# Performance work log

Measured on AMD Instinct MI355X. Metric: run time of the kernel, lower is better.

Reference implementation:

```python
import jax, jax.numpy as jnp
import numpy as np

D_MODEL = 256
MLP_DIM = 1024
EPS = 1e-5

def _layernorm(x, g, b):
    mu = jnp.mean(x, axis=-1, keepdims=True)
    var = jnp.mean(jnp.square(x - mu), axis=-1, keepdims=True)
    return (x - mu) * jax.lax.rsqrt(var + EPS) * g + b

def setup_inputs() -> dict:
    key = jax.random.key(0)
    ks = jax.random.split(key, 4)
    d, m = D_MODEL, MLP_DIM
    x = jax.random.normal(ks[0], (8, 1024, 4, d), dtype=jnp.float32)
    w_qkv = jax.random.normal(ks[1], (3 * d, d), dtype=jnp.float32) * 0.05  # torch Linear weight (out,in)
    gamma1 = jnp.ones((d,), jnp.float32)
    beta1 = jnp.zeros((d,), jnp.float32)
    gamma2 = jnp.ones((d,), jnp.float32)
    beta2 = jnp.zeros((d,), jnp.float32)
    w1 = jax.random.normal(ks[2], (m, d), dtype=jnp.float32) * 0.05
    b1 = jnp.zeros((m,), jnp.float32)
    w2 = jax.random.normal(ks[3], (d, m), dtype=jnp.float32) * 0.05
    b2 = jnp.zeros((d,), jnp.float32)
    return {"x": x, "w_qkv": w_qkv, "gamma1": gamma1, "beta1": beta1,
            "gamma2": gamma2, "beta2": beta2, "w1": w1, "b1": b1, "w2": w2, "b2": b2}

def reference(x, w_qkv, gamma1, beta1, gamma2, beta2, w1, b1, w2, b2):
    bsz, n, h, d = x.shape
    scale = d ** -0.5
    # --- attention branch: x + attn(norm1(x)) ---
    xn = _layernorm(x, gamma1, beta1)
    # Linear(d, 3d): xn @ W^T, then reshape trailing 3d -> (d, 3) as in torch
    qkv = jnp.einsum('bnhd,ed->bnhe', xn, w_qkv).reshape(bsz, n * h, d, 3)
    q, k, v = qkv[..., 0], qkv[..., 1], qkv[..., 2]   # [b, n*h, d]
    dots = jnp.einsum('bid,bjd->bij', q, k) * scale   # [b, n*h, n*h]
    attn = jax.nn.softmax(dots, axis=-1)              # dropout=0 -> identity
    out = jnp.einsum('bij,bjd->bid', attn, v).reshape(bsz, n, h, d)
    x = x + out
    # --- mlp branch: x + mlp(norm2(x)) ---
    xn2 = _layernorm(x, gamma2, beta2)
    hid = jax.nn.silu(jnp.einsum('bnhd,md->bnhm', xn2, w1) + b1)
    x = x + jnp.einsum('bnhm,dm->bnhd', hid, w2) + b2
    return x
```

## Files before the change

### kernel.cpp

```cpp
#include <hip/hip_runtime.h>


typedef __attribute__((ext_vector_type(8))) short bf16x8;
typedef __attribute__((ext_vector_type(4))) short bf16x4;
typedef __attribute__((ext_vector_type(4))) float f32x4;
typedef __attribute__((ext_vector_type(16))) float f32x16;

static __device__ __forceinline__ short f2bf(float f) {
    union { float f; unsigned u; } v; v.f = f;
    unsigned r = (v.u + 0x7FFFu + ((v.u >> 16) & 1u)) >> 16;
    return (short)r;
}

static __device__ __forceinline__ void gll16(const void* g, void* l) {
    __builtin_amdgcn_global_load_lds(
        (const __attribute__((address_space(1))) unsigned*)g,
        (__attribute__((address_space(3))) unsigned*)l, 16, 0, 0);
}

__global__ __launch_bounds__(256) void k_cvt(const float* __restrict__ wqkv,
                                             const float* __restrict__ w1,
                                             const float* __restrict__ w2,
                                             short* __restrict__ owqkv,
                                             short* __restrict__ ow1,
                                             short* __restrict__ ow2) {
    int i = blockIdx.x * 256 + threadIdx.x;
    if (i < 196608) {
        int e = i >> 8, col = i & 255;
        int dd = e / 3, which = e - dd * 3;
        float v = wqkv[i];
        if (which == 0) v *= 0.0625f * 1.44269504f;
        owqkv[((which << 8) + dd) * 256 + col] = f2bf(v);
    }
    if (i < 262144) { ow1[i] = f2bf(w1[i]); ow2[i] = f2bf(w2[i]); }
}

__global__ __launch_bounds__(256) void k_ln(const float* __restrict__ x,
                                            const float* __restrict__ g,
                                            const float* __restrict__ bta,
                                            short* __restrict__ out) {
    int w = threadIdx.x >> 6, lane = threadIdx.x & 63;
    long row = (long)blockIdx.x * 4 + w;
    float4 v = *((const float4*)(x + row * 256) + lane);
    float s = v.x + v.y + v.z + v.w;
    float q = v.x * v.x + v.y * v.y + v.z * v.z + v.w * v.w;
    for (int off = 1; off < 64; off <<= 1) {
        s += __shfl_xor(s, off);
        q += __shfl_xor(q, off);
    }
    float mean = s * (1.0f / 256.0f);
    float var = q * (1.0f / 256.0f) - mean * mean;
    float rstd = rsqrtf(var + 1e-5f);
    float4 gg = *((const float4*)g + lane);
    float4 bb = *((const float4*)bta + lane);
    short4 o;
    o.x = f2bf((v.x - mean) * rstd * gg.x + bb.x);
    o.y = f2bf((v.y - mean) * rstd * gg.y + bb.y);
    o.z = f2bf((v.z - mean) * rstd * gg.z + bb.z);
    o.w = f2bf((v.w - mean) * rstd * gg.w + bb.w);
    *((short4*)(out + row * 256) + lane) = o;
}

__global__ __launch_bounds__(512, 2) void k_qkv(const short* __restrict__ xn,
                                                const short* __restrict__ wb,
                                                short* __restrict__ Q,
                                                short* __restrict__ K,
                                                short* __restrict__ VT) {
    __shared__ __attribute__((aligned(16))) short lds_b[2][64 * 256];
    __shared__ __attribute__((aligned(16))) short lds_t[64 * 136];
    int t = threadIdx.x, w = t >> 6, l = t & 63, l5 = l & 31;
    int ln = l & 15, qd = l >> 4;
    int m0 = blockIdx.x * 128;
    int moff = (w >> 1) * 32, noff = (w & 1) * 32;

    bf16x8 af[2][8];
    #pragma unroll
    for (int mi = 0; mi < 2; mi++)
        #pragma unroll
        for (int kc = 0; kc < 8; kc++)
            af[mi][kc] = *(const bf16x8*)(xn + (long)(m0 + moff + mi * 16 + ln) * 256 + kc * 32 + qd * 8);

    int boff[4], blds[4];
    #pragma unroll
    for (int i = 0; i < 4; i++) {
        int r = w * 8 + i * 2 + (l >> 5);
        boff[i] = r * 512 + ((l5 ^ (r & 31)) * 16);
        blds[i] = (w * 8 + i * 2) * 512;
    }
    const char* gB = (const char*)wb;
    #pragma unroll
    for (int i = 0; i < 4; i++) gll16(gB + boff[i], (char*)lds_b[0] + blds[i]);
    __syncthreads();

    for (int nt = 0; nt < 12; nt++) {
        int cur = nt & 1;
        if (nt < 11) {
            long base = (long)(nt + 1) * 32768;
            #pragma unroll
            for (int i = 0; i < 4; i++)
                gll16(gB + base + boff[i], (char*)lds_b[cur ^ 1] + blds[i]);
        }
        const char* lb = (const char*)lds_b[cur];
        f32x4 acc[2][2] = {};
        #pragma unroll
        for (int ks = 0; ks < 8; ks++) {
            int ca = ks * 4 + qd;
            int rb0 = noff + ln, rb1 = noff + 16 + ln;
            bf16x8 b0 = *(const bf16x8*)(lb + rb0 * 512 + ((ca ^ (rb0 & 31)) * 16));
            bf16x8 b1 = *(const bf16x8*)(lb + rb1 * 512 + ((ca ^ (rb1 & 31)) * 16));
            acc[0][0] = __builtin_amdgcn_mfma_f32_16x16x32_bf16(af[0][ks], b0, acc[0][0], 0, 0, 0);
            acc[0][1] = __builtin_amdgcn_mfma_f32_16x16x32_bf16(af[0][ks], b1, acc[0][1], 0, 0, 0);
            acc[1][0] = __builtin_amdgcn_mfma_f32_16x16x32_bf16(af[1][ks], b0, acc[1][0], 0, 0, 0);
            acc[1][1] = __builtin_amdgcn_mfma_f32_16x16x32_bf16(af[1][ks], b1, acc[1][1], 0, 0, 0);
        }
        int e0 = nt * 64;
        if (e0 < 512) {
            #pragma unroll
            for (int mi = 0; mi < 2; mi++)
                #pragma unroll
                for (int nj = 0; nj < 2; nj++)
                    #pragma unroll
                    for (int rg = 0; rg < 4; rg++) {
                        int gr = m0 + moff + mi * 16 + qd * 4 + rg;
                        int e = e0 + noff + nj * 16 + ln;
                        short bv = f2bf(acc[mi][nj][rg]);
                        if (e < 256) Q[(long)gr * 256 + e] = bv;
                        else K[(long)gr * 256 + (e - 256)] = bv;
                    }
        } else {
            #pragma unroll
            for (int mi = 0; mi < 2; mi++)
                #pragma unroll
                for (int nj = 0; nj < 2; nj++)
                    #pragma unroll
                    for (int rg = 0; rg < 4; rg++) {
                        int dl = noff + nj * 16 + ln;
                        int il = moff + mi * 16 + qd * 4 + rg;
                        lds_t[dl * 136 + il] = f2bf(acc[mi][nj][rg]);
                    }
            __syncthreads();
            int bb = m0 >> 12, i0 = m0 & 4095;
            int dl = t >> 3, ch = t & 7;
            const int4* s4 = (const int4*)(lds_t + dl * 136 + ch * 16);
            int4 v0 = s4[0], v1 = s4[1];
            long vrow = ((long)(bb * 256 + (e0 - 512) + dl)) * 4096 + i0 + ch * 16;
            *(int4*)(VT + vrow) = v0;
            *(int4*)(VT + vrow + 8) = v1;
        }
        __syncthreads();
    }
}

__global__ __launch_bounds__(512, 2) void k_attn(const short* __restrict__ Q,
                                                 const short* __restrict__ K,
                                                 const short* __restrict__ VT,
                                                 const float* __restrict__ x,
                                                 float* __restrict__ out) {
    __shared__ __attribute__((aligned(16))) short lds_k[2][64 * 256];
    __shared__ __attribute__((aligned(16))) short lds_v[2][2][256 * 40];
    int t = threadIdx.x, w = t >> 6, l = t & 63, l5 = l & 31, h = l >> 5;
    int ww = w & 3, hkv = w >> 2;
    int b = blockIdx.x;
    int q0 = blockIdx.y * 128 + ww * 32;

    bf16x8 qf[16];
    {
        const short* qrow = Q + ((long)(b * 4096 + q0 + l5)) * 256;
        #pragma unroll
        for (int kc = 0; kc < 16; kc++) qf[kc] = *(const bf16x8*)(qrow + kc * 16 + h * 8);
    }
    f32x16 O[8] = {};
    float lsum = 0.f;

    const char* Kb = (const char*)(K + (long)b * 4096 * 256);
    const int4* gv = (const int4*)(VT + (long)b * 4096 * 256);

    int koff[4], klds[4];
    #pragma unroll
    for (int i = 0; i < 4; i++) {
        int r = w * 8 + i * 2 + (l >> 5);
        koff[i] = r * 512 + ((l5 ^ (r & 31)) * 16);
        klds[i] = (w * 8 + i * 2) * 512;
    }
    int vgbase[4], vloff[4];
    #pragma unroll
    for (int i = 0; i < 4; i++) {
        int c = t + 512 * i;
        int sub = c >> 10, cc = c & 1023, d = cc >> 2, ch = cc & 3;
        vgbase[i] = d * 512 + sub * 4 + ch;
        vloff[i] = sub * 20480 + d * 80 + ch * 16;
    }
    int4 vs[4];

    #pragma unroll
    for (int i = 0; i < 4; i++) vs[i] = gv[vgbase[i]];
    #pragma unroll
    for (int i = 0; i < 4; i++) gll16(Kb + koff[i], (char*)lds_k[0] + klds[i]);
    #pragma unroll
    for (int i = 0; i < 4; i++)
        *(int4*)((char*)lds_v + vloff[i]) = vs[i];
    __syncthreads();

    const char* lvmine = (const char*)lds_v + hkv * 20480;

    for (int jt = 0; jt < 64; jt++) {
        int cur = jt & 1;
        if (jt < 63) {
            #pragma unroll
            for (int i = 0; i < 4; i++) vs[i] = gv[vgbase[i] + (jt + 1) * 8];
            int ka = (jt + 1) * 32768;
            #pragma unroll
            for (int i = 0; i < 4; i++)
                gll16(Kb + ka + koff[i], (char*)lds_k[cur ^ 1] + klds[i]);
        }
        const short* lk = lds_k[cur] + hkv * 32 * 256;
        const char* lv = lvmine + cur * 40960;
        f32x16 st = {};
        #pragma unroll
        for (int kc = 0; kc < 16; kc++) {
            int cc = kc * 2 + h;
            bf16x8 a = *(const bf16x8*)(lk + (l5 * 32 + (cc ^ l5)) * 8);
            st = __builtin_amdgcn_mfma_f32_32x32x16_bf16(a, qf[kc], st, 0, 0, 0);
        }
        unsigned pw[4][2];
        #pragma unroll
        for (int r4 = 0; r4 < 4; r4++) {
            float p0 = __builtin_amdgcn_exp2f(st[r4 * 4 + 0]);
            float p1 = __builtin_amdgcn_exp2f(st[r4 * 4 + 1]);
            float p2 = __builtin_amdgcn_exp2f(st[r4 * 4 + 2]);
            float p3 = __builtin_amdgcn_exp2f(st[r4 * 4 + 3]);
            lsum += (p0 + p1) + (p2 + p3);
            union { float f; unsigned u; } u0, u1, u2, u3;
            u0.f = p0; u1.f = p1; u2.f = p2; u3.f = p3;
            pw[r4][0] = __builtin_amdgcn_perm(u1.u + 0x8000u, u0.u + 0x8000u, 0x07060302u);
            pw[r4][1] = __builtin_amdgcn_perm(u3.u + 0x8000u, u2.u + 0x8000u, 0x07060302u);
        }
        bf16x8 pfr[2];
        #pragma unroll
        for (int k2 = 0; k2 < 2; k2++) {
            unsigned a0 = pw[2 * k2][0], a1 = pw[2 * k2][1];
            unsigned b0 = pw[2 * k2 + 1][0], b1 = pw[2 * k2 + 1][1];
            asm("v_permlane32_swap_b32 %0, %1" : "+v"(a0), "+v"(b0));
            asm("v_permlane32_swap_b32 %0, %1" : "+v"(a1), "+v"(b1));
            union { unsigned u[4]; bf16x8 v; } f;
            f.u[0] = a0; f.u[1] = a1; f.u[2] = b0; f.u[3] = b1;
            pfr[k2] = f.v;
        }
        if (jt < 63) {
            #pragma unroll
            for (int i = 0; i < 4; i++)
                *(int4*)((char*)lds_v + (cur ^ 1) * 40960 + vloff[i]) = vs[i];
        }
        #pragma unroll
        for (int dt = 0; dt < 8; dt++) {
            const char* vbase = lv + (dt * 32 + l5) * 80;
            #pragma unroll
            for (int k2 = 0; k2 < 2; k2++) {
                bf16x8 va = *(const bf16x8*)(vbase + (k2 * 2 + h) * 16);
                O[dt] = __builtin_amdgcn_mfma_f32_32x32x16_bf16(va, pfr[k2], O[dt], 0, 0, 0);
            }
        }
        __syncthreads();
    }

    float lt = lsum + __shfl_xor(lsum, 32);
    float* lmrg = (float*)&lds_v[1][0][0];
    lmrg[hkv * 128 + ww * 32 + l5] = lt;
    __syncthreads();
    float ltot = lmrg[ww * 32 + l5] + lmrg[128 + ww * 32 + l5];
    float rinv = 1.0f / ltot;

    float* omrg = (float*)&lds_v[0][0][0];
    float* fscr = (float*)lds_k[0] + ww * (32 * 33);
    #pragma unroll
    for (int dt = 0; dt < 8; dt++) {
        if (hkv == 1) {
            #pragma unroll
            for (int r = 0; r < 16; r++) omrg[ww * 1024 + r * 64 + l] = O[dt][r];
        }
        __syncthreads();
        if (hkv == 0) {
            #pragma unroll
            for (int r = 0; r < 16; r++) {
                float Om = O[dt][r] + omrg[ww * 1024 + r * 64 + l];
                int drow = (r & 3) + 8 * (r >> 2) + 4 * h;
                fscr[drow * 33 + l5] = Om * rinv;
            }
            asm volatile("s_waitcnt lgkmcnt(0)" ::: "memory");
            #pragma unroll
            for (int it = 0; it < 16; it++) {
                int ql = it * 2 + h;
                float v = fscr[l5 * 33 + ql];
                long idx = ((long)(b * 4096 + q0 + ql)) * 256 + dt * 32 + l5;
                out[idx] = x[idx] + v;
            }
            asm volatile("s_waitcnt lgkmcnt(0)" ::: "memory");
        }
        __syncthreads();
    }
}

__global__ __launch_bounds__(256, 2) void k_mlp(const short* __restrict__ xn,
                                                const short* __restrict__ w1b,
                                                const short* __restrict__ w2b,
                                                const float* __restrict__ b1,
                                                const float* __restrict__ b2,
                                                float* __restrict__ out) {
    __shared__ __attribute__((aligned(16))) short lds_w[2][32 * 256];
    __shared__ __attribute__((aligned(16))) short lds_h[64 * 264];
    int t = threadIdx.x, w = t >> 6, l = t & 63, l5 = l & 31, ln = l & 15, qd = l >> 4;
    int R0 = blockIdx.x * 64;
    int mrow = (w & 1) * 32, colh = (w >> 1) * 16;
    int lr = colh + ln;

    long s1off[4], s2off[4]; int wlds[4];
    #pragma unroll
    for (int i = 0; i < 4; i++) {
        int r = w * 8 + i * 2 + (l >> 5);
        int ch = l5 ^ (r & 31);
        s1off[i] = (long)r * 512 + ch * 16;
        s2off[i] = (long)r * 2048 + ch * 16;
        wlds[i] = (w * 8 + i * 2) * 512;
    }
    const char* W1c = (const char*)w1b;
    const char* W2c = (const char*)w2b;

    f32x4 Oc[8][2] = {};
    #pragma unroll
    for (int i = 0; i < 4; i++)
        gll16(W1c + s1off[i], (char*)lds_w[0] + wlds[i]);
    __syncthreads();
    int cur = 0;

    for (int pass = 0; pass < 4; pass++) {
        bf16x8 a1f[2][8];
        #pragma unroll
        for (int mi = 0; mi < 2; mi++)
            #pragma unroll
            for (int kc = 0; kc < 8; kc++)
                a1f[mi][kc] = *(const bf16x8*)(xn + (long)(R0 + mrow + mi * 16 + ln) * 256 + kc * 32 + qd * 8);
        #pragma unroll
        for (int nt = 0; nt < 8; nt++) {
            if (nt < 7) {
                long base = (long)(pass * 256 + (nt + 1) * 32) * 512;
                #pragma unroll
                for (int i = 0; i < 4; i++)
                    gll16(W1c + base + s1off[i], (char*)lds_w[cur ^ 1] + wlds[i]);
            } else {
                long base = (long)pass * 512;
                #pragma unroll
                for (int i = 0; i < 4; i++)
                    gll16(W2c + base + s2off[i], (char*)lds_w[cur ^ 1] + wlds[i]);
            }
            const short* lw = lds_w[cur];
            f32x4 acc[2] = {};
            #pragma unroll
            for (int kc = 0; kc < 8; kc++) {
                int cc = kc * 4 + qd;
                bf16x8 bf = *(const bf16x8*)(lw + lr * 256 + (cc ^ lr) * 8);
                acc[0] = __builtin_amdgcn_mfma_f32_16x16x32_bf16(a1f[0][kc], bf, acc[0], 0, 0, 0);
                acc[1] = __builtin_amdgcn_mfma_f32_16x16x32_bf16(a1f[1][kc], bf, acc[1], 0, 0, 0);
            }
            float bb = b1[pass * 256 + nt * 32 + lr];
            #pragma unroll
            for (int mi = 0; mi < 2; mi++)
                #pragma unroll
                for (int rg = 0; rg < 4; rg++) {
                    float z = acc[mi][rg] + bb;
                    float sv = z / (1.0f + __expf(-z));
                    lds_h[(mrow + mi * 16 + qd * 4 + rg) * 264 + nt * 32 + lr] = f2bf(sv);
                }
            __syncthreads();
            cur ^= 1;
        }
        bf16x8 a2f[2][8];
        #pragma unroll
        for (int mi = 0; mi < 2; mi++)
            #pragma unroll
            for (int kc = 0; kc < 8; kc++)
                a2f[mi][kc] = *(const bf16x8*)&lds_h[(mrow + mi * 16 + ln) * 264 + kc * 32 + qd * 8];
        #pragma unroll
        for (int nt = 0; nt < 8; nt++) {
            if (nt < 7) {
                long base = (long)((nt + 1) * 32) * 2048 + (long)pass * 512;
                #pragma unroll
                for (int i = 0; i < 4; i++)
                    gll16(W2c + base + s2off[i], (char*)lds_w[cur ^ 1] + wlds[i]);
            } else if (pass < 3) {
                long base = (long)((pass + 1) * 256) * 512;
                #pragma unroll
                for (int i = 0; i < 4; i++)
                    gll16(W1c + base + s1off[i], (char*)lds_w[cur ^ 1] + wlds[i]);
            }
            const short* lw = lds_w[cur];
            #pragma unroll
            for (int kc = 0; kc < 8; kc++) {
                int cc = kc * 4 + qd;
                bf16x8 bf = *(const bf16x8*)(lw + lr * 256 + (cc ^ lr) * 8);
                Oc[nt][0] = __builtin_amdgcn_mfma_f32_16x16x32_bf16(a2f[0][kc], bf, Oc[nt][0], 0, 0, 0);
                Oc[nt][1] = __builtin_amdgcn_mfma_f32_16x16x32_bf16(a2f[1][kc], bf, Oc[nt][1], 0, 0, 0);
            }
            __syncthreads();
            cur ^= 1;
        }
    }
    #pragma unroll
    for (int nt = 0; nt < 8; nt++) {
        int dd = nt * 32 + lr;
        float bb = b2[dd];
        #pragma unroll
        for (int mi = 0; mi < 2; mi++)
            #pragma unroll
            for (int rg = 0; rg < 4; rg++) {
                long idx = (long)(R0 + mrow + mi * 16 + qd * 4 + rg) * 256 + dd;
                out[idx] = out[idx] + Oc[nt][mi][rg] + bb;
            }
    }
}

extern "C" void kernel_launch(void* const* d_in, const int* in_sizes, int n_in,
                              void* d_out, int out_size, void* d_ws, size_t ws_size,
                              hipStream_t stream) {
    const float* x    = (const float*)d_in[0];
    const float* wqkv = (const float*)d_in[1];
    const float* g1   = (const float*)d_in[2];
    const float* be1  = (const float*)d_in[3];
    const float* g2   = (const float*)d_in[4];
    const float* be2  = (const float*)d_in[5];
    const float* w1   = (const float*)d_in[6];
    const float* b1   = (const float*)d_in[7];
    const float* w2   = (const float*)d_in[8];
    const float* b2   = (const float*)d_in[9];
    float* out = (float*)d_out;
    char* ws = (char*)d_ws;
    short* WQKV = (short*)(ws);
    short* W1B  = (short*)(ws + (512l << 10));
    short* W2B  = (short*)(ws + (1l << 20));
    short* XN   = (short*)(ws + (2l << 20));
    short* Qb   = (short*)(ws + (18l << 20));
    short* Kb   = (short*)(ws + (34l << 20));
    short* VTb  = (short*)(ws + (50l << 20));

    k_cvt<<<1024, 256, 0, stream>>>(wqkv, w1, w2, WQKV, W1B, W2B);
    k_ln<<<8192, 256, 0, stream>>>(x, g1, be1, XN);
    k_qkv<<<256, 512, 0, stream>>>(XN, WQKV, Qb, Kb, VTb);
    k_attn<<<dim3(8, 32), 512, 0, stream>>>(Qb, Kb, VTb, x, out);
    k_ln<<<8192, 256, 0, stream>>>(out, g2, be2, XN);
    k_mlp<<<512, 256, 0, stream>>>(XN, W1B, W2B, b1, b2, out);
}
```

Baseline: 399.3 us.

## Fuse layernorms into QKV and MLP kernels, drop standalone LN launches

Removes the two k_ln kernels and the bf16 normalized-activation buffer. The QKV and MLP kernels now read fp32 rows directly, compute mean and rstd per row with cross-lane shuffles, and build the bf16 A-fragments in registers. The intent is to cut two launches and the write-then-read of the normalized tensor. In exchange each GEMM block reads fp32 input twice (stats pass, then normalize pass) and uses more registers. The MLP A-fragments are also loaded once before the pass loop instead of once per pass.

Result: slower. 415.2 us (+4.0%).

```diff
diff --git a/kernel.cpp b/kernel.cpp
--- a/kernel.cpp
+++ b/kernel.cpp
@@ -16,6 +16,55 @@
     __builtin_amdgcn_global_load_lds(
         (const __attribute__((address_space(1))) unsigned*)g,
         (__attribute__((address_space(3))) unsigned*)l, 16, 0, 0);
+}
+
+static __device__ __forceinline__ void ln_frags(const float* __restrict__ xin,
+                                                const float* __restrict__ g,
+                                                const float* __restrict__ be,
+                                                long r0, int ln, int qd,
+                                                bf16x8 af[2][8]) {
+    float mean[2], rstd[2];
+    #pragma unroll
+    for (int mi = 0; mi < 2; mi++) {
+        const float* xr = xin + (r0 + mi * 16 + ln) * 256 + qd * 8;
+        float s = 0.f, qq = 0.f;
+        #pragma unroll
+        for (int kc = 0; kc < 8; kc++) {
+            float4 lo = *(const float4*)(xr + kc * 32);
+            float4 hi = *(const float4*)(xr + kc * 32 + 4);
+            s += (lo.x + lo.y) + (lo.z + lo.w) + (hi.x + hi.y) + (hi.z + hi.w);
+            qq += lo.x * lo.x + lo.y * lo.y + lo.z * lo.z + lo.w * lo.w
+                + hi.x * hi.x + hi.y * hi.y + hi.z * hi.z + hi.w * hi.w;
+        }
+        s += __shfl_xor(s, 16); s += __shfl_xor(s, 32);
+        qq += __shfl_xor(qq, 16); qq += __shfl_xor(qq, 32);
+        mean[mi] = s * (1.0f / 256.0f);
+        float var = qq * (1.0f / 256.0f) - mean[mi] * mean[mi];
+        rstd[mi] = rsqrtf(var + 1e-5f);
+    }
+    #pragma unroll
+    for (int mi = 0; mi < 2; mi++) {
+        const float* xr = xin + (r0 + mi * 16 + ln) * 256 + qd * 8;
+        #pragma unroll
+        for (int kc = 0; kc < 8; kc++) {
+            float4 lo = *(const float4*)(xr + kc * 32);
+            float4 hi = *(const float4*)(xr + kc * 32 + 4);
+            float4 glo = *(const float4*)(g + kc * 32 + qd * 8);
+            float4 ghi = *(const float4*)(g + kc * 32 + qd * 8 + 4);
+            float4 blo = *(const float4*)(be + kc * 32 + qd * 8);
+            float4 bhi = *(const float4*)(be + kc * 32 + qd * 8 + 4);
+            union { short s[8]; bf16x8 v; } pk;
+            pk.s[0] = f2bf((lo.x - mean[mi]) * rstd[mi] * glo.x + blo.x);
+            pk.s[1] = f2bf((lo.y - mean[mi]) * rstd[mi] * glo.y + blo.y);
+            pk.s[2] = f2bf((lo.z - mean[mi]) * rstd[mi] * glo.z + blo.z);
+            pk.s[3] = f2bf((lo.w - mean[mi]) * rstd[mi] * glo.w + blo.w);
+            pk.s[4] = f2bf((hi.x - mean[mi]) * rstd[mi] * ghi.x + bhi.x);
+            pk.s[5] = f2bf((hi.y - mean[mi]) * rstd[mi] * ghi.y + bhi.y);
+            pk.s[6] = f2bf((hi.z - mean[mi]) * rstd[mi] * ghi.z + bhi.z);
+            pk.s[7] = f2bf((hi.w - mean[mi]) * rstd[mi] * ghi.w + bhi.w);
+            af[mi][kc] = pk.v;
+        }
+    }
 }
 
 __global__ __launch_bounds__(256) void k_cvt(const float* __restrict__ wqkv,
@@ -35,33 +84,9 @@
     if (i < 262144) { ow1[i] = f2bf(w1[i]); ow2[i] = f2bf(w2[i]); }
 }
 
-__global__ __launch_bounds__(256) void k_ln(const float* __restrict__ x,
-                                            const float* __restrict__ g,
-                                            const float* __restrict__ bta,
-                                            short* __restrict__ out) {
-    int w = threadIdx.x >> 6, lane = threadIdx.x & 63;
-    long row = (long)blockIdx.x * 4 + w;
-    float4 v = *((const float4*)(x + row * 256) + lane);
-    float s = v.x + v.y + v.z + v.w;
-    float q = v.x * v.x + v.y * v.y + v.z * v.z + v.w * v.w;
-    for (int off = 1; off < 64; off <<= 1) {
-        s += __shfl_xor(s, off);
-        q += __shfl_xor(q, off);
-    }
-    float mean = s * (1.0f / 256.0f);
-    float var = q * (1.0f / 256.0f) - mean * mean;
-    float rstd = rsqrtf(var + 1e-5f);
-    float4 gg = *((const float4*)g + lane);
-    float4 bb = *((const float4*)bta + lane);
-    short4 o;
-    o.x = f2bf((v.x - mean) * rstd * gg.x + bb.x);
-    o.y = f2bf((v.y - mean) * rstd * gg.y + bb.y);
-    o.z = f2bf((v.z - mean) * rstd * gg.z + bb.z);
-    o.w = f2bf((v.w - mean) * rstd * gg.w + bb.w);
-    *((short4*)(out + row * 256) + lane) = o;
-}
-
-__global__ __launch_bounds__(512, 2) void k_qkv(const short* __restrict__ xn,
+__global__ __launch_bounds__(512, 2) void k_qkv(const float* __restrict__ x,
+                                                const float* __restrict__ g1,
+                                                const float* __restrict__ be1,
                                                 const short* __restrict__ wb,
                                                 short* __restrict__ Q,
                                                 short* __restrict__ K,
@@ -73,13 +98,6 @@
     int m0 = blockIdx.x * 128;
     int moff = (w >> 1) * 32, noff = (w & 1) * 32;
 
-    bf16x8 af[2][8];
-    #pragma unroll
-    for (int mi = 0; mi < 2; mi++)
-        #pragma unroll
-        for (int kc = 0; kc < 8; kc++)
-            af[mi][kc] = *(const bf16x8*)(xn + (long)(m0 + moff + mi * 16 + ln) * 256 + kc * 32 + qd * 8);
-
     int boff[4], blds[4];
     #pragma unroll
     for (int i = 0; i < 4; i++) {
@@ -90,6 +108,9 @@
     const char* gB = (const char*)wb;
     #pragma unroll
     for (int i = 0; i < 4; i++) gll16(gB + boff[i], (char*)lds_b[0] + blds[i]);
+
+    bf16x8 af[2][8];
+    ln_frags(x, g1, be1, (long)(m0 + moff), ln, qd, af);
     __syncthreads();
 
     for (int nt = 0; nt < 12; nt++) {
@@ -300,7 +321,9 @@
     }
 }
 
-__global__ __launch_bounds__(256, 2) void k_mlp(const short* __restrict__ xn,
+__global__ __launch_bounds__(256, 2) void k_mlp(const float* __restrict__ xin,
+                                                const float* __restrict__ g2,
+                                                const float* __restrict__ be2,
                                                 const short* __restrict__ w1b,
                                                 const short* __restrict__ w2b,
                                                 const float* __restrict__ b1,
@@ -325,20 +348,17 @@
     const char* W1c = (const char*)w1b;
     const char* W2c = (const char*)w2b;
 
-    f32x4 Oc[8][2] = {};
     #pragma unroll
     for (int i = 0; i < 4; i++)
         gll16(W1c + s1off[i], (char*)lds_w[0] + wlds[i]);
+
+    bf16x8 a1f[2][8];
+    ln_frags(xin, g2, be2, (long)(R0 + mrow), ln, qd, a1f);
     __syncthreads();
     int cur = 0;
 
+    f32x4 Oc[8][2] = {};
     for (int pass = 0; pass < 4; pass++) {
-        bf16x8 a1f[2][8];
-        #pragma unroll
-        for (int mi = 0; mi < 2; mi++)
-            #pragma unroll
-            for (int kc = 0; kc < 8; kc++)
-                a1f[mi][kc] = *(const bf16x8*)(xn + (long)(R0 + mrow + mi * 16 + ln) * 256 + kc * 32 + qd * 8);
         #pragma unroll
         for (int nt = 0; nt < 8; nt++) {
             if (nt < 7) {
@@ -436,15 +456,12 @@
     short* WQKV = (short*)(ws);
     short* W1B  = (short*)(ws + (512l << 10));
     short* W2B  = (short*)(ws + (1l << 20));
-    short* XN   = (short*)(ws + (2l << 20));
     short* Qb   = (short*)(ws + (18l << 20));
     short* Kb   = (short*)(ws + (34l << 20));
     short* VTb  = (short*)(ws + (50l << 20));
 
     k_cvt<<<1024, 256, 0, stream>>>(wqkv, w1, w2, WQKV, W1B, W2B);
-    k_ln<<<8192, 256, 0, stream>>>(x, g1, be1, XN);
-    k_qkv<<<256, 512, 0, stream>>>(XN, WQKV, Qb, Kb, VTb);
+    k_qkv<<<256, 512, 0, stream>>>(x, g1, be1, WQKV, Qb, Kb, VTb);
     k_attn<<<dim3(8, 32), 512, 0, stream>>>(Qb, Kb, VTb, x, out);
-    k_ln<<<8192, 256, 0, stream>>>(out, g2, be2, XN);
-    k_mlp<<<512, 256, 0, stream>>>(XN, W1B, W2B, b1, b2, out);
-}
+    k_mlp<<<512, 256, 0, stream>>>(out, g2, be2, W1B, W2B, b1, b2, out);
+}
```
